# Kernel optimization log

Measured on AMD Instinct MI355X. Metric: run time of the kernel, lower is better.

The kernel has to match this reference:

```python
import jax, jax.numpy as jnp
import numpy as np

_EPS = 1e-8
TEMPERATURE = 0.1  # head_cfg.temperature
WEIGHT = 1.0       # float(head_cfg.weight[1:]) with weight='w1'
N = 100000
K = 31   # nsample - 1
C = 64
NUM_CLASSES = 17


def setup_inputs() -> dict:
    key = jax.random.key(0)
    k1, k2, k3 = jax.random.split(key, 3)
    features = jax.random.normal(k1, (N, C), dtype=jnp.float32)
    labels = jax.random.randint(k2, (N,), 0, NUM_CLASSES, dtype=jnp.int32)
    # KNN neighbor indices with self excluded (original drops idx[...,1:]);
    # offset trick guarantees neighbor_idx[i, j] != i.
    off = jax.random.randint(k3, (N, K), 1, N, dtype=jnp.int32)
    neighbor_idx = (jnp.arange(N, dtype=jnp.int32)[:, None] + off) % N
    return {"features": features, "labels": labels, "neighbor_idx": neighbor_idx}


def reference(features, labels, neighbor_idx):
    # posmask_cnt: argmax of one-hot labels == integer class-id comparison
    neighbor_label = labels[neighbor_idx]                      # (N, K) int
    posmask = labels[:, None] == neighbor_label                # (N, K) bool
    cnt = posmask.sum(axis=1)
    point_mask = (cnt > 0) & (cnt < K)                          # (N,) bool

    # dist_l2 on gathered neighbor features
    neighbor_feature = features[neighbor_idx]                  # (N, K, C)
    diff = features[:, None, :] - neighbor_feature             # (N, K, C)
    dist = jnp.sqrt(jnp.sum(diff * diff, axis=-1)) + _EPS      # (N, K)

    # contrast_softnn
    logits = -dist
    logits = logits - jnp.max(logits, axis=1, keepdims=True)
    logits = logits / TEMPERATURE
    exp = jnp.exp(logits)                                      # (N, K)
    pos = jnp.sum(exp * posmask, axis=1)
    neg = jnp.sum(exp, axis=1)
    loss = -jnp.log(pos / neg + _EPS)                          # (N,)

    # masked mean == torch.mean(loss[point_mask])
    pm = point_mask.astype(loss.dtype)
    denom = jnp.maximum(jnp.sum(pm), 1.0)
    return jnp.sum(loss * pm) / denom * WEIGHT
```

## Files before the change

kernel.cpp:

```cpp
#include <hip/hip_runtime.h>
#include <hip/hip_fp16.h>

#define KNB 31
#define CH 64
#define TEMP_INV 10.0f

typedef _Float16 h2 __attribute__((ext_vector_type(2)));
typedef float f2 __attribute__((ext_vector_type(2)));


__global__ void ch_init_ws(double* __restrict__ ws, unsigned* __restrict__ ctr) {
    ws[0] = 0.0;
    ws[1] = 0.0;
    *ctr  = 0u;
}

__global__ __launch_bounds__(256) void ch_cvt8(
    const float* __restrict__ in, unsigned char* __restrict__ out,
    double* __restrict__ ws, int total8)
{
    const int idx = blockIdx.x * blockDim.x + threadIdx.x;
    if (idx == 0) { ws[0] = 0.0; ws[1] = 0.0; }
    if (idx >= total8) return;
    const float4* ip = reinterpret_cast<const float4*>(in) + (size_t)idx * 2;
    const float4 a = ip[0];
    const float4 b = ip[1];
    unsigned lo = 0u, hi = 0u;
    lo = __builtin_amdgcn_cvt_pk_fp8_f32(a.x, a.y, lo, false);
    lo = __builtin_amdgcn_cvt_pk_fp8_f32(a.z, a.w, lo, true);
    hi = __builtin_amdgcn_cvt_pk_fp8_f32(b.x, b.y, hi, false);
    hi = __builtin_amdgcn_cvt_pk_fp8_f32(b.z, b.w, hi, true);
    uint2 o; o.x = lo; o.y = hi;
    reinterpret_cast<uint2*>(out)[idx] = o;
}

__global__ __launch_bounds__(256) void ch_main8q(
    const unsigned char* __restrict__ tab8,
    const int*           __restrict__ labels,
    const int*           __restrict__ nidx,
    double*              __restrict__ ws,
    int n)
{
    const int t   = threadIdx.x;
    const int i   = blockIdx.x * (256 / 4) + (t >> 2);
    const int sub = t & 3;

    float loss_w = 0.0f;
    float pm_f   = 0.0f;

    if (i < n) {
        float fA[16];
        {
            union { uint4 u; unsigned w[4]; } Au;
            Au.u = reinterpret_cast<const uint4*>(tab8 + (size_t)i * CH)[sub];
            #pragma unroll
            for (int q = 0; q < 4; ++q) {
                const f2 p0 = __builtin_amdgcn_cvt_pk_f32_fp8(Au.w[q], false);
                const f2 p1 = __builtin_amdgcn_cvt_pk_f32_fp8(Au.w[q], true);
                fA[4 * q + 0] = p0[0]; fA[4 * q + 1] = p0[1];
                fA[4 * q + 2] = p1[0]; fA[4 * q + 3] = p1[1];
            }
        }

        const int lab = labels[i];
        const int* nrow = nidx + (size_t)i * KNB;

        float m  = -1e30f;
        float se = 0.0f;
        float sp = 0.0f;
        int   cnt = 0;

        #pragma unroll 4
        for (int j = 0; j < KNB; ++j) {
            const int nj = nrow[j];

            union { uint4 u; unsigned w[4]; } Bu;
            Bu.u = reinterpret_cast<const uint4*>(tab8 + (size_t)nj * CH)[sub];

            float s = 0.0f;
            #pragma unroll
            for (int q = 0; q < 4; ++q) {
                const f2 p0 = __builtin_amdgcn_cvt_pk_f32_fp8(Bu.w[q], false);
                const f2 p1 = __builtin_amdgcn_cvt_pk_f32_fp8(Bu.w[q], true);
                float d;
                d = fA[4 * q + 0] - p0[0]; s = fmaf(d, d, s);
                d = fA[4 * q + 1] - p0[1]; s = fmaf(d, d, s);
                d = fA[4 * q + 2] - p1[0]; s = fmaf(d, d, s);
                d = fA[4 * q + 3] - p1[1]; s = fmaf(d, d, s);
            }
            s += __shfl_xor(s, 1);
            s += __shfl_xor(s, 2);

            const float l = -(sqrtf(s) + 1e-8f);
            const bool pm = (labels[nj] == lab);
            cnt += pm ? 1 : 0;

            if (l > m) {
                const float r = __expf((m - l) * TEMP_INV);
                se *= r;
                sp *= r;
                m = l;
            }
            const float e = __expf((l - m) * TEMP_INV);
            se += e;
            if (pm) sp += e;
        }

        if (sub == 0 && cnt > 0 && cnt < KNB) {
            loss_w = -logf(sp / se + 1e-8f);
            pm_f   = 1.0f;
        }
    }

    __shared__ float s_l[256];
    __shared__ float s_c[256];
    s_l[t] = loss_w;
    s_c[t] = pm_f;
    __syncthreads();
    #pragma unroll
    for (int off = 128; off > 0; off >>= 1) {
        if (t < off) {
            s_l[t] += s_l[t + off];
            s_c[t] += s_c[t + off];
        }
        __syncthreads();
    }
    if (t == 0) {
        atomicAdd(ws,     (double)s_l[0]);
        atomicAdd(ws + 1, (double)s_c[0]);
    }
}

__global__ __launch_bounds__(256) void ch_cvt(
    const float* __restrict__ in, __half* __restrict__ out, int total8)
{
    const int idx = blockIdx.x * blockDim.x + threadIdx.x;
    if (idx >= total8) return;
    const float4* ip = reinterpret_cast<const float4*>(in) + (size_t)idx * 2;
    const float4 a = ip[0];
    const float4 b = ip[1];
    union { uint4 u; __half2 h[4]; } o;
    o.h[0] = __floats2half2_rn(a.x, a.y);
    o.h[1] = __floats2half2_rn(a.z, a.w);
    o.h[2] = __floats2half2_rn(b.x, b.y);
    o.h[3] = __floats2half2_rn(b.z, b.w);
    reinterpret_cast<uint4*>(out)[idx] = o.u;
}

__device__ __forceinline__ float dot2acc(h2 d, float s) {
    return __builtin_amdgcn_fdot2(d, d, s, false);
}

template <bool FP16>
__global__ __launch_bounds__(256) void ch_main4(
    const float*  __restrict__ feat,
    const __half* __restrict__ tab,
    const int*    __restrict__ labels,
    const int*    __restrict__ nidx,
    double*       __restrict__ ws,
    int n)
{
    const int t   = threadIdx.x;
    const int i   = blockIdx.x * (256 / 4) + (t >> 2);
    const int sub = t & 3;

    float loss_w = 0.0f;
    float pm_f   = 0.0f;

    if (i < n) {
        float f[16];
        union { uint4 u[2]; h2 h[8]; } A;
        if constexpr (FP16) {
            const uint4* ap = reinterpret_cast<const uint4*>(tab + (size_t)i * CH + sub * 16);
            A.u[0] = ap[0];
            A.u[1] = ap[1];
        } else {
            const float4* ap = reinterpret_cast<const float4*>(feat + (size_t)i * CH + sub * 16);
            #pragma unroll
            for (int q = 0; q < 4; ++q) {
                const float4 v = ap[q];
                f[4 * q]     = v.x;
                f[4 * q + 1] = v.y;
                f[4 * q + 2] = v.z;
                f[4 * q + 3] = v.w;
            }
        }

        const int lab = labels[i];
        float m = -1e30f, se = 0.0f, sp = 0.0f;
        int cnt = 0;

        #pragma unroll 2
        for (int j = 0; j < KNB; ++j) {
            const int nj = nidx[(size_t)i * KNB + j];

            float s = 0.0f;
            if constexpr (FP16) {
                union { uint4 u[2]; h2 h[8]; } B;
                const uint4* bp = reinterpret_cast<const uint4*>(tab + (size_t)nj * CH + sub * 16);
                B.u[0] = bp[0];
                B.u[1] = bp[1];
                #pragma unroll
                for (int q = 0; q < 8; ++q) {
                    const h2 d = A.h[q] - B.h[q];
                    s = dot2acc(d, s);
                }
            } else {
                const float4* bp = reinterpret_cast<const float4*>(feat + (size_t)nj * CH + sub * 16);
                #pragma unroll
                for (int q = 0; q < 4; ++q) {
                    const float4 v = bp[q];
                    const float dx = f[4 * q]     - v.x;
                    const float dy = f[4 * q + 1] - v.y;
                    const float dz = f[4 * q + 2] - v.z;
                    const float dw = f[4 * q + 3] - v.w;
                    s += dx * dx + dy * dy + dz * dz + dw * dw;
                }
            }
            s += __shfl_xor(s, 1);
            s += __shfl_xor(s, 2);

            const float l = -(sqrtf(s) + 1e-8f);
            const bool pm = (labels[nj] == lab);
            cnt += pm ? 1 : 0;

            if (l > m) {
                const float r = __expf((m - l) * TEMP_INV);
                se *= r; sp *= r; m = l;
            }
            const float e = __expf((l - m) * TEMP_INV);
            se += e;
            if (pm) sp += e;
        }

        if (sub == 0 && cnt > 0 && cnt < KNB) {
            loss_w = -logf(sp / se + 1e-8f);
            pm_f   = 1.0f;
        }
    }

    __shared__ float s_l[256];
    __shared__ float s_c[256];
    s_l[t] = loss_w;
    s_c[t] = pm_f;
    __syncthreads();
    #pragma unroll
    for (int off = 128; off > 0; off >>= 1) {
        if (t < off) {
            s_l[t] += s_l[t + off];
            s_c[t] += s_c[t + off];
        }
        __syncthreads();
    }
    if (t == 0) {
        atomicAdd(ws,     (double)s_l[0]);
        atomicAdd(ws + 1, (double)s_c[0]);
    }
}

__global__ void ch_finalize(const double* __restrict__ ws, float* __restrict__ out) {
    double c = ws[1];
    if (c < 1.0) c = 1.0;
    out[0] = (float)(ws[0] / c);
}

extern "C" void kernel_launch(void* const* d_in, const int* in_sizes, int n_in,
                              void* d_out, int out_size, void* d_ws, size_t ws_size,
                              hipStream_t stream) {
    const float* feat   = (const float*)d_in[0];
    const int*   labels = (const int*)d_in[1];
    const int*   nidx   = (const int*)d_in[2];
    float*       out    = (float*)d_out;
    double*      ws     = (double*)d_ws;
    unsigned*    ctr    = (unsigned*)((char*)d_ws + 16);

    const int n = in_sizes[1];
    const int total8 = n * CH / 8;

    if (ws_size >= 256 + (size_t)n * CH) {
        unsigned char* tab = (unsigned char*)d_ws + 256;
        ch_cvt8<<<(total8 + 255) / 256, 256, 0, stream>>>(feat, tab, ws, total8);
        const int blocks = (n + 63) / 64;
        ch_main8q<<<blocks, 256, 0, stream>>>(tab, labels, nidx, ws, n);
        ch_finalize<<<1, 1, 0, stream>>>(ws, out);
        return;
    }

    ch_init_ws<<<1, 1, 0, stream>>>(ws, ctr);
    const int blocks = (n + 63) / 64;
    if (ws_size >= 256 + (size_t)n * CH * 2) {
        __half* tab = reinterpret_cast<__half*>((char*)d_ws + 256);
        ch_cvt<<<(total8 + 255) / 256, 256, 0, stream>>>(feat, tab, total8);
        ch_main4<true><<<blocks, 256, 0, stream>>>(feat, tab, labels, nidx, ws, n);
    } else {
        ch_main4<false><<<blocks, 256, 0, stream>>>(feat, nullptr, labels, nidx, ws, n);
    }
    ch_finalize<<<1, 1, 0, stream>>>(ws, out);
}
```

Measured before the change: 79.47 us.

## Split neighbor gather into two passes over table halves for cache locality

The main loss kernel is split into two kernels. The first processes only neighbors whose index falls in the lower half of the fp8 feature table and saves per-point online-softmax state (max, sum, positive sum, count) to workspace. The second processes the upper-half neighbors and then reduces the loss. Each pass then randomly gathers from a smaller working set (about 3.2MB instead of 6.4MB), which may fit better in L2 or MALL. The cost is reading the neighbor index row and the point's own features twice, warp divergence on the half check, an extra state round trip, and one more kernel launch. The unused fp16 path is also removed.

```diff
diff --git a/kernel.cpp b/kernel.cpp
--- a/kernel.cpp
+++ b/kernel.cpp
@@ -9,10 +9,9 @@
 typedef float f2 __attribute__((ext_vector_type(2)));
 
 
-__global__ void ch_init_ws(double* __restrict__ ws, unsigned* __restrict__ ctr) {
+__global__ void ch_init_ws(double* __restrict__ ws) {
     ws[0] = 0.0;
     ws[1] = 0.0;
-    *ctr  = 0u;
 }
 
 __global__ __launch_bounds__(256) void ch_cvt8(
@@ -34,12 +33,85 @@
     reinterpret_cast<uint2*>(out)[idx] = o;
 }
 
-__global__ __launch_bounds__(256) void ch_main8q(
+__global__ __launch_bounds__(256) void ch_mainA(
     const unsigned char* __restrict__ tab8,
     const int*           __restrict__ labels,
     const int*           __restrict__ nidx,
+    float4*              __restrict__ state,
+    int n, int nhalf)
+{
+    const int t   = threadIdx.x;
+    const int i   = blockIdx.x * (256 / 4) + (t >> 2);
+    const int sub = t & 3;
+    if (i >= n) return;
+
+    float fA[16];
+    {
+        union { uint4 u; unsigned w[4]; } Au;
+        Au.u = reinterpret_cast<const uint4*>(tab8 + (size_t)i * CH)[sub];
+        #pragma unroll
+        for (int q = 0; q < 4; ++q) {
+            const f2 p0 = __builtin_amdgcn_cvt_pk_f32_fp8(Au.w[q], false);
+            const f2 p1 = __builtin_amdgcn_cvt_pk_f32_fp8(Au.w[q], true);
+            fA[4 * q + 0] = p0[0]; fA[4 * q + 1] = p0[1];
+            fA[4 * q + 2] = p1[0]; fA[4 * q + 3] = p1[1];
+        }
+    }
+
+    const int lab = labels[i];
+    const int* nrow = nidx + (size_t)i * KNB;
+
+    float m  = -1e30f;
+    float se = 0.0f;
+    float sp = 0.0f;
+    int   cnt = 0;
+
+    #pragma unroll 4
+    for (int j = 0; j < KNB; ++j) {
+        const int nj = nrow[j];
+        if (nj < nhalf) {
+            union { uint4 u; unsigned w[4]; } Bu;
+            Bu.u = reinterpret_cast<const uint4*>(tab8 + (size_t)nj * CH)[sub];
+
+            float s = 0.0f;
+            #pragma unroll
+            for (int q = 0; q < 4; ++q) {
+                const f2 p0 = __builtin_amdgcn_cvt_pk_f32_fp8(Bu.w[q], false);
+                const f2 p1 = __builtin_amdgcn_cvt_pk_f32_fp8(Bu.w[q], true);
+                float d;
+                d = fA[4 * q + 0] - p0[0]; s = fmaf(d, d, s);
+                d = fA[4 * q + 1] - p0[1]; s = fmaf(d, d, s);
+                d = fA[4 * q + 2] - p1[0]; s = fmaf(d, d, s);
+                d = fA[4 * q + 3] - p1[1]; s = fmaf(d, d, s);
+            }
+            s += __shfl_xor(s, 1);
+            s += __shfl_xor(s, 2);
+
+            const float l = -(sqrtf(s) + 1e-8f);
+            const bool pm = (labels[nj] == lab);
+            cnt += pm ? 1 : 0;
+
+            if (l > m) {
+                const float r = __expf((m - l) * TEMP_INV);
+                se *= r; sp *= r; m = l;
+            }
+            const float e = __expf((l - m) * TEMP_INV);
+            se += e;
+            if (pm) sp += e;
+        }
+    }
+
+    if (sub == 0)
+        state[i] = make_float4(m, se, sp, (float)cnt);
+}
+
+__global__ __launch_bounds__(256) void ch_mainB(
+    const unsigned char* __restrict__ tab8,
+    const int*           __restrict__ labels,
+    const int*           __restrict__ nidx,
+    const float4*        __restrict__ state,
     double*              __restrict__ ws,
-    int n)
+    int n, int nhalf)
 {
     const int t   = threadIdx.x;
     const int i   = blockIdx.x * (256 / 4) + (t >> 2);
@@ -65,6 +137,103 @@
         const int lab = labels[i];
         const int* nrow = nidx + (size_t)i * KNB;
 
+        const float4 st = state[i];
+        float m  = st.x;
+        float se = st.y;
+        float sp = st.z;
+        int   cnt = (int)st.w;
+
+        #pragma unroll 4
+        for (int j = 0; j < KNB; ++j) {
+            const int nj = nrow[j];
+            if (nj >= nhalf) {
+                union { uint4 u; unsigned w[4]; } Bu;
+                Bu.u = reinterpret_cast<const uint4*>(tab8 + (size_t)nj * CH)[sub];
+
+                float s = 0.0f;
+                #pragma unroll
+                for (int q = 0; q < 4; ++q) {
+                    const f2 p0 = __builtin_amdgcn_cvt_pk_f32_fp8(Bu.w[q], false);
+                    const f2 p1 = __builtin_amdgcn_cvt_pk_f32_fp8(Bu.w[q], true);
+                    float d;
+                    d = fA[4 * q + 0] - p0[0]; s = fmaf(d, d, s);
+                    d = fA[4 * q + 1] - p0[1]; s = fmaf(d, d, s);
+                    d = fA[4 * q + 2] - p1[0]; s = fmaf(d, d, s);
+                    d = fA[4 * q + 3] - p1[1]; s = fmaf(d, d, s);
+                }
+                s += __shfl_xor(s, 1);
+                s += __shfl_xor(s, 2);
+
+                const float l = -(sqrtf(s) + 1e-8f);
+                const bool pm = (labels[nj] == lab);
+                cnt += pm ? 1 : 0;
+
+                if (l > m) {
+                    const float r = __expf((m - l) * TEMP_INV);
+                    se *= r; sp *= r; m = l;
+                }
+                const float e = __expf((l - m) * TEMP_INV);
+                se += e;
+                if (pm) sp += e;
+            }
+        }
+
+        if (sub == 0 && cnt > 0 && cnt < KNB) {
+            loss_w = -logf(sp / se + 1e-8f);
+            pm_f   = 1.0f;
+        }
+    }
+
+    __shared__ float s_l[256];
+    __shared__ float s_c[256];
+    s_l[t] = loss_w;
+    s_c[t] = pm_f;
+    __syncthreads();
+    #pragma unroll
+    for (int off = 128; off > 0; off >>= 1) {
+        if (t < off) {
+            s_l[t] += s_l[t + off];
+            s_c[t] += s_c[t + off];
+        }
+        __syncthreads();
+    }
+    if (t == 0) {
+        atomicAdd(ws,     (double)s_l[0]);
+        atomicAdd(ws + 1, (double)s_c[0]);
+    }
+}
+
+__global__ __launch_bounds__(256) void ch_main8q(
+    const unsigned char* __restrict__ tab8,
+    const int*           __restrict__ labels,
+    const int*           __restrict__ nidx,
+    double*              __restrict__ ws,
+    int n)
+{
+    const int t   = threadIdx.x;
+    const int i   = blockIdx.x * (256 / 4) + (t >> 2);
+    const int sub = t & 3;
+
+    float loss_w = 0.0f;
+    float pm_f   = 0.0f;
+
+    if (i < n) {
+        float fA[16];
+        {
+            union { uint4 u; unsigned w[4]; } Au;
+            Au.u = reinterpret_cast<const uint4*>(tab8 + (size_t)i * CH)[sub];
+            #pragma unroll
+            for (int q = 0; q < 4; ++q) {
+                const f2 p0 = __builtin_amdgcn_cvt_pk_f32_fp8(Au.w[q], false);
+                const f2 p1 = __builtin_amdgcn_cvt_pk_f32_fp8(Au.w[q], true);
+                fA[4 * q + 0] = p0[0]; fA[4 * q + 1] = p0[1];
+                fA[4 * q + 2] = p1[0]; fA[4 * q + 3] = p1[1];
+            }
+        }
+
+        const int lab = labels[i];
+        const int* nrow = nidx + (size_t)i * KNB;
+
         float m  = -1e30f;
         float se = 0.0f;
         float sp = 0.0f;
@@ -97,9 +266,7 @@
 
             if (l > m) {
                 const float r = __expf((m - l) * TEMP_INV);
-                se *= r;
-                sp *= r;
-                m = l;
+                se *= r; sp *= r; m = l;
             }
             const float e = __expf((l - m) * TEMP_INV);
             se += e;
@@ -131,33 +298,11 @@
     }
 }
 
-__global__ __launch_bounds__(256) void ch_cvt(
-    const float* __restrict__ in, __half* __restrict__ out, int total8)
-{
-    const int idx = blockIdx.x * blockDim.x + threadIdx.x;
-    if (idx >= total8) return;
-    const float4* ip = reinterpret_cast<const float4*>(in) + (size_t)idx * 2;
-    const float4 a = ip[0];
-    const float4 b = ip[1];
-    union { uint4 u; __half2 h[4]; } o;
-    o.h[0] = __floats2half2_rn(a.x, a.y);
-    o.h[1] = __floats2half2_rn(a.z, a.w);
-    o.h[2] = __floats2half2_rn(b.x, b.y);
-    o.h[3] = __floats2half2_rn(b.z, b.w);
-    reinterpret_cast<uint4*>(out)[idx] = o.u;
-}
-
-__device__ __forceinline__ float dot2acc(h2 d, float s) {
-    return __builtin_amdgcn_fdot2(d, d, s, false);
-}
-
-template <bool FP16>
-__global__ __launch_bounds__(256) void ch_main4(
-    const float*  __restrict__ feat,
-    const __half* __restrict__ tab,
-    const int*    __restrict__ labels,
-    const int*    __restrict__ nidx,
-    double*       __restrict__ ws,
+__global__ __launch_bounds__(256) void ch_main4f(
+    const float* __restrict__ feat,
+    const int*   __restrict__ labels,
+    const int*   __restrict__ nidx,
+    double*      __restrict__ ws,
     int n)
 {
     const int t   = threadIdx.x;
@@ -169,61 +314,34 @@
 
     if (i < n) {
         float f[16];
-        union { uint4 u[2]; h2 h[8]; } A;
-        if constexpr (FP16) {
-            const uint4* ap = reinterpret_cast<const uint4*>(tab + (size_t)i * CH + sub * 16);
-            A.u[0] = ap[0];
-            A.u[1] = ap[1];
-        } else {
-            const float4* ap = reinterpret_cast<const float4*>(feat + (size_t)i * CH + sub * 16);
-            #pragma unroll
-            for (int q = 0; q < 4; ++q) {
-                const float4 v = ap[q];
-                f[4 * q]     = v.x;
-                f[4 * q + 1] = v.y;
-                f[4 * q + 2] = v.z;
-                f[4 * q + 3] = v.w;
-            }
-        }
-
+        const float4* ap = reinterpret_cast<const float4*>(feat + (size_t)i * CH + sub * 16);
+        #pragma unroll
+        for (int q = 0; q < 4; ++q) {
+            const float4 v = ap[q];
+            f[4 * q] = v.x; f[4 * q + 1] = v.y; f[4 * q + 2] = v.z; f[4 * q + 3] = v.w;
+        }
         const int lab = labels[i];
         float m = -1e30f, se = 0.0f, sp = 0.0f;
         int cnt = 0;
-
         #pragma unroll 2
         for (int j = 0; j < KNB; ++j) {
             const int nj = nidx[(size_t)i * KNB + j];
-
+            const float4* bp = reinterpret_cast<const float4*>(feat + (size_t)nj * CH + sub * 16);
             float s = 0.0f;
-            if constexpr (FP16) {
-                union { uint4 u[2]; h2 h[8]; } B;
-                const uint4* bp = reinterpret_cast<const uint4*>(tab + (size_t)nj * CH + sub * 16);
-                B.u[0] = bp[0];
-                B.u[1] = bp[1];
-                #pragma unroll
-                for (int q = 0; q < 8; ++q) {
-                    const h2 d = A.h[q] - B.h[q];
-                    s = dot2acc(d, s);
-                }
-            } else {
-                const float4* bp = reinterpret_cast<const float4*>(feat + (size_t)nj * CH + sub * 16);
-                #pragma unroll
-                for (int q = 0; q < 4; ++q) {
-                    const float4 v = bp[q];
-                    const float dx = f[4 * q]     - v.x;
-                    const float dy = f[4 * q + 1] - v.y;
-                    const float dz = f[4 * q + 2] - v.z;
-                    const float dw = f[4 * q + 3] - v.w;
-                    s += dx * dx + dy * dy + dz * dz + dw * dw;
-                }
+            #pragma unroll
+            for (int q = 0; q < 4; ++q) {
+                const float4 v = bp[q];
+                float d;
+                d = f[4 * q]     - v.x; s += d * d;
+                d = f[4 * q + 1] - v.y; s += d * d;
+                d = f[4 * q + 2] - v.z; s += d * d;
+                d = f[4 * q + 3] - v.w; s += d * d;
             }
             s += __shfl_xor(s, 1);
             s += __shfl_xor(s, 2);
-
             const float l = -(sqrtf(s) + 1e-8f);
             const bool pm = (labels[nj] == lab);
             cnt += pm ? 1 : 0;
-
             if (l > m) {
                 const float r = __expf((m - l) * TEMP_INV);
                 se *= r; sp *= r; m = l;
@@ -232,7 +350,6 @@
             se += e;
             if (pm) sp += e;
         }
-
         if (sub == 0 && cnt > 0 && cnt < KNB) {
             loss_w = -logf(sp / se + 1e-8f);
             pm_f   = 1.0f;
@@ -272,28 +389,34 @@
     const int*   nidx   = (const int*)d_in[2];
     float*       out    = (float*)d_out;
     double*      ws     = (double*)d_ws;
-    unsigned*    ctr    = (unsigned*)((char*)d_ws + 16);
 
     const int n = in_sizes[1];
     const int total8 = n * CH / 8;
-
-    if (ws_size >= 256 + (size_t)n * CH) {
+    const int blocks = (n + 63) / 64;
+
+    const size_t tab_bytes   = (size_t)n * CH;
+    const size_t state_bytes = (size_t)n * 16;
+
+    if (ws_size >= 256 + tab_bytes + state_bytes) {
+        unsigned char* tab = (unsigned char*)d_ws + 256;
+        float4* state = reinterpret_cast<float4*>((char*)d_ws + 256 + tab_bytes);
+        const int nhalf = n / 2;
+        ch_cvt8<<<(total8 + 255) / 256, 256, 0, stream>>>(feat, tab, ws, total8);
+        ch_mainA<<<blocks, 256, 0, stream>>>(tab, labels, nidx, state, n, nhalf);
+        ch_mainB<<<blocks, 256, 0, stream>>>(tab, labels, nidx, state, ws, n, nhalf);
+        ch_finalize<<<1, 1, 0, stream>>>(ws, out);
+        return;
+    }
+
+    if (ws_size >= 256 + tab_bytes) {
         unsigned char* tab = (unsigned char*)d_ws + 256;
         ch_cvt8<<<(total8 + 255) / 256, 256, 0, stream>>>(feat, tab, ws, total8);
-        const int blocks = (n + 63) / 64;
         ch_main8q<<<blocks, 256, 0, stream>>>(tab, labels, nidx, ws, n);
         ch_finalize<<<1, 1, 0, stream>>>(ws, out);
         return;
     }
 
-    ch_init_ws<<<1, 1, 0, stream>>>(ws, ctr);
-    const int blocks = (n + 63) / 64;
-    if (ws_size >= 256 + (size_t)n * CH * 2) {
-        __half* tab = reinterpret_cast<__half*>((char*)d_ws + 256);
-        ch_cvt<<<(total8 + 255) / 256, 256, 0, stream>>>(feat, tab, total8);
-        ch_main4<true><<<blocks, 256, 0, stream>>>(feat, tab, labels, nidx, ws, n);
-    } else {
-        ch_main4<false><<<blocks, 256, 0, stream>>>(feat, nullptr, labels, nidx, ws, n);
-    }
+    ch_init_ws<<<1, 1, 0, stream>>>(ws);
+    ch_main4f<<<blocks, 256, 0, stream>>>(feat, labels, nidx, ws, n);
     ch_finalize<<<1, 1, 0, stream>>>(ws, out);
 }
```

New measurement: 121.2 us. 52.5% more time.
